# Optimization experiments

Measured on AMD Instinct MI355X. Metric: run time of the kernel, lower is better.

Reference implementation:

```python
import jax, jax.numpy as jnp
import numpy as np

# dims: B batch, N seq, D model_dim, R lora rank, C codebooks, K codebook_input_channel, P kv pairs, M per-codebook output
B, N, D, R, C, K, P = 4, 2048, 1024, 8, 64, 16, 64
M = (D * R) // C  # 128


def setup_inputs() -> dict:
    key = jax.random.key(0)
    ks = jax.random.split(key, 7)
    x = jax.random.normal(ks[0], (B, N, D), dtype=jnp.float32)
    W_A = jax.random.normal(ks[1], (C, K, D), dtype=jnp.float32) * (D ** -0.5)
    emb_A = jax.random.uniform(ks[2], (C, P, K), dtype=jnp.float32, minval=-1.5, maxval=1.5)
    vals_A = jax.random.normal(ks[3], (C, P, M), dtype=jnp.float32)
    W_B = jax.random.normal(ks[4], (C, K, D), dtype=jnp.float32) * (D ** -0.5)
    emb_B = jax.random.uniform(ks[5], (C, P, K), dtype=jnp.float32, minval=-1.5, maxval=1.5)
    vals_B = jax.random.normal(ks[6], (C, P, M), dtype=jnp.float32)
    return {"x": x, "W_A": W_A, "emb_A": emb_A, "vals_A": vals_A,
            "W_B": W_B, "emb_B": emb_B, "vals_B": vals_B}


def _discrete_kv(x, W, emb, vals):
    # x: [B,N,D]; W: [C,K,D] (Linear weight per codebook); emb: [C,P,K]; vals: [C,P,M]
    proj = jnp.einsum('bnd,ckd->cbnk', x, W)  # per-codebook linear projection
    # squared euclidean distance to each key (argmin is same as cdist argmin)
    d2 = (jnp.sum(proj * proj, axis=-1, keepdims=True)
          - 2.0 * jnp.einsum('cbnk,cpk->cbnp', proj, emb)
          + jnp.sum(emb * emb, axis=-1)[:, None, None, :])  # [C,B,N,P]
    idx = jnp.argmin(d2, axis=-1)                      # [C,B,N]
    y = jax.vmap(lambda v, i: v[i])(vals, idx)          # [C,B,N,M]
    # concat over codebooks on last dim -> [B,N,C*M], then view as [B,N,R,D]
    return jnp.transpose(y, (1, 2, 0, 3)).reshape(x.shape[0], x.shape[1], R, D)


def reference(x, W_A, emb_A, vals_A, W_B, emb_B, vals_B):
    A = _discrete_kv(x, W_A, emb_A, vals_A)   # [B,N,R,D]
    Bm = _discrete_kv(x, W_B, emb_B, vals_B)  # [B,N,R,D]
    t = jnp.einsum('bnd,bnrd->bnr', x, A)
    return jnp.einsum('bnr,bnrd->bnd', t, Bm)
```

## Files before the change

kernel.cpp:

```cpp
#include <hip/hip_runtime.h>

#define NTOK   8192
#define DMODEL 1024
#define NC     64
#define NK     16
#define NP     64
#define NM     128
#define LCAP   (1 << 18)
#define MARGIN 2e-3f

typedef _Float16 f16x8  __attribute__((ext_vector_type(8)));
typedef float    f32x16 __attribute__((ext_vector_type(16)));

#define AS1 __attribute__((address_space(1)))
#define AS3 __attribute__((address_space(3)))

__device__ __forceinline__ void glds16(const void* g, void* l) {
    __builtin_amdgcn_global_load_lds((const AS1 void*)g, (AS3 void*)l, 16, 0, 0);
}

__global__ __launch_bounds__(256) void k_split(
    const float* __restrict__ x, const float* __restrict__ W_A, const float* __restrict__ W_B,
    short* __restrict__ xh, short* __restrict__ xl,
    short* __restrict__ whA, short* __restrict__ wlA,
    short* __restrict__ whB, short* __restrict__ wlB)
{
    const int t = blockIdx.x * 256 + threadIdx.x;
    const int NX = 128 * NTOK;
    const int NW = 128 * 1024;

    const float* src;
    short *dh, *dl;
    if (t < NX) {
        const int chunk = t >> 13, tok = t & 8191;
        src = x + (size_t)tok * DMODEL + chunk * 8;
        dh = xh + (size_t)t * 8;  dl = xl + (size_t)t * 8;
    } else if (t < NX + NW) {
        const int u = t - NX, chunk = u >> 10, ck = u & 1023;
        src = W_A + (size_t)ck * DMODEL + chunk * 8;
        dh = whA + (size_t)u * 8; dl = wlA + (size_t)u * 8;
    } else {
        const int u = t - NX - NW, chunk = u >> 10, ck = u & 1023;
        src = W_B + (size_t)ck * DMODEL + chunk * 8;
        dh = whB + (size_t)u * 8; dl = wlB + (size_t)u * 8;
    }

    const float4 a = *(const float4*)src;
    const float4 b = *(const float4*)(src + 4);
    const float v[8] = {a.x, a.y, a.z, a.w, b.x, b.y, b.z, b.w};
    unsigned h[8], l[8];
    #pragma unroll
    for (int j = 0; j < 8; ++j) {
        const _Float16 hf = (_Float16)v[j];
        const _Float16 lf = (_Float16)(v[j] - (float)hf);
        h[j] = (unsigned)__builtin_bit_cast(unsigned short, hf);
        l[j] = (unsigned)__builtin_bit_cast(unsigned short, lf);
    }
    *(int4*)dh = make_int4((int)(h[0] | (h[1] << 16)), (int)(h[2] | (h[3] << 16)),
                           (int)(h[4] | (h[5] << 16)), (int)(h[6] | (h[7] << 16)));
    *(int4*)dl = make_int4((int)(l[0] | (l[1] << 16)), (int)(l[2] | (l[3] << 16)),
                           (int)(l[4] | (l[5] << 16)), (int)(l[6] | (l[7] << 16)));
}

__global__ __launch_bounds__(512, 1) void k_mfma_argmin(
    const short* __restrict__ xh, const short* __restrict__ xl,
    const short* __restrict__ whA, const short* __restrict__ wlA,
    const short* __restrict__ whB, const short* __restrict__ wlB,
    const float* __restrict__ emb_A, const float* __restrict__ emb_B,
    int* __restrict__ idxbuf, int* __restrict__ list, int* __restrict__ cnt)
{
    __shared__ __align__(16) float smem[32768];
    short* ls = (short*)smem;
    float* projT = smem;
    float* embS  = smem + 16640;
    float* e2S   = smem + 24832;

    const int tid = threadIdx.x;
    const int bid = blockIdx.x;
    const int swz = (bid & 7) * 32 + (bid >> 3);
    const int tb  = swz >> 3;
    const int ot  = swz & 7;
    const int set = ot >> 2;
    const short* __restrict__ wh = set ? whB : whA;
    const short* __restrict__ wl = set ? wlB : wlA;
    const float* __restrict__ Ep = set ? emb_B : emb_A;
    const int ckbase = (ot & 3) * 256;

    const int lane = tid & 63;
    const int wid  = tid >> 6;
    const int wr   = wid >> 2;
    const int wc   = wid & 3;
    const int lr31 = lane & 31;
    const int lk2  = lane >> 5;

    f32x16 acc[4][2];
    #pragma unroll
    for (int m = 0; m < 4; ++m)
        #pragma unroll
        for (int n = 0; n < 2; ++n)
            #pragma unroll
            for (int r = 0; r < 16; ++r) acc[m][n][r] = 0.f;

    const size_t oA = ((size_t)(tid >> 8) * NTOK + tb * 256 + (tid & 255)) * 8;
    const size_t oB = ((size_t)(tid >> 8) * 1024 + ckbase + (tid & 255)) * 8;

    #define STAGE(buf, st)                                                   \
        do {                                                                 \
            const size_t sa_ = (size_t)(st) * (size_t)(2 * NTOK * 8);        \
            const size_t sb_ = (size_t)(st) * (size_t)(2 * 1024 * 8);        \
            short* lb_ = ls + (buf) * 16384 + tid * 8;                       \
            glds16(xh + oA + sa_, lb_);                                      \
            glds16(xl + oA + sa_, lb_ + 4096);                               \
            glds16(wh + oB + sb_, lb_ + 8192);                               \
            glds16(wl + oB + sb_, lb_ + 12288);                              \
        } while (0)

    const int aoff = (lk2 * 256 + wr * 128 + lr31) * 8;
    const int boff = 8192 + (lk2 * 256 + wc * 64 + lr31) * 8;

    STAGE(0, 0);
    STAGE(1, 1);
    STAGE(2, 2);

    for (int t = 0; t < 64; ++t) {
        asm volatile("s_waitcnt vmcnt(8)" ::: "memory");
        __builtin_amdgcn_s_barrier();

        const short* bb = ls + (t & 3) * 16384;
        f16x8 ah[4], al[4], bh[2], bl[2];
        #pragma unroll
        for (int m = 0; m < 4; ++m) {
            ah[m] = *(const f16x8*)(bb + aoff + m * 256);
            al[m] = *(const f16x8*)(bb + 4096 + aoff + m * 256);
        }
        #pragma unroll
        for (int n = 0; n < 2; ++n) {
            bh[n] = *(const f16x8*)(bb + boff + n * 256);
            bl[n] = *(const f16x8*)(bb + 8192 - 8192 + 12288 - 12288 + 4096 + boff + n * 256);
        }

        {
            const int ts = (t + 3 < 64) ? (t + 3) : 63;
            STAGE((t + 3) & 3, ts);
        }

        asm volatile("s_waitcnt lgkmcnt(0)" ::: "memory");
        __builtin_amdgcn_sched_barrier(0);
        __builtin_amdgcn_s_setprio(1);
        #pragma unroll
        for (int m = 0; m < 4; ++m)
            #pragma unroll
            for (int n = 0; n < 2; ++n) {
                acc[m][n] = __builtin_amdgcn_mfma_f32_32x32x16_f16(ah[m], bh[n], acc[m][n], 0, 0, 0);
                acc[m][n] = __builtin_amdgcn_mfma_f32_32x32x16_f16(ah[m], bl[n], acc[m][n], 0, 0, 0);
                acc[m][n] = __builtin_amdgcn_mfma_f32_32x32x16_f16(al[m], bh[n], acc[m][n], 0, 0, 0);
            }
        __builtin_amdgcn_s_setprio(0);
    }
    #undef STAGE

    asm volatile("s_waitcnt vmcnt(0)" ::: "memory");
    __builtin_amdgcn_s_barrier();

    #pragma unroll
    for (int ch = 0; ch < 2; ++ch) {
        __syncthreads();
        {
            const float4* eg = (const float4*)(Ep + (size_t)((ot & 3) * 16 + ch * 8) * NP * NK);
            float4* es = (float4*)embS;
            #pragma unroll
            for (int i = 0; i < 4; ++i) es[tid + 512 * i] = eg[tid + 512 * i];
        }
        __syncthreads();
        {
            const float* e = embS + tid * 16;
            float s = 0.f;
            #pragma unroll
            for (int k = 0; k < 16; ++k) s = fmaf(e[k], e[k], s);
            e2S[tid] = s;
        }
        #pragma unroll
        for (int c = 0; c < 4; ++c) {
            __syncthreads();
            if (wr == (c >> 1)) {
                #pragma unroll
                for (int mi = 0; mi < 2; ++mi) {
                    const int m = (c & 1) * 2 + mi;
                    #pragma unroll
                    for (int n = 0; n < 2; ++n) {
                        const int col = wc * 64 + n * 32 + lr31;
                        #pragma unroll
                        for (int r = 0; r < 16; ++r) {
                            const int trow = mi * 32 + (r & 3) + 8 * (r >> 2) + 4 * lk2;
                            projT[col * 65 + trow] = acc[m][n][r];
                        }
                    }
                }
            }
            __syncthreads();
            {
                const int lt = tid & 63, cbl = tid >> 6;
                float pr[16];
                #pragma unroll
                for (int k = 0; k < 16; ++k)
                    pr[k] = projT[((ch * 8 + cbl) * 16 + k) * 65 + lt];
                const float4* eb4 = (const float4*)(embS + cbl * 1024);
                const float* e2 = e2S + cbl * 64;
                float best = 1e30f, second = 1e30f;
                int bp = 0;
                for (int p = 0; p < 64; ++p) {
                    const float4 e0 = eb4[p * 4 + 0], e1 = eb4[p * 4 + 1];
                    const float4 e2v = eb4[p * 4 + 2], e3 = eb4[p * 4 + 3];
                    float s = 0.f;
                    s = fmaf(pr[0], e0.x, s);   s = fmaf(pr[1], e0.y, s);
                    s = fmaf(pr[2], e0.z, s);   s = fmaf(pr[3], e0.w, s);
                    s = fmaf(pr[4], e1.x, s);   s = fmaf(pr[5], e1.y, s);
                    s = fmaf(pr[6], e1.z, s);   s = fmaf(pr[7], e1.w, s);
                    s = fmaf(pr[8], e2v.x, s);  s = fmaf(pr[9], e2v.y, s);
                    s = fmaf(pr[10], e2v.z, s); s = fmaf(pr[11], e2v.w, s);
                    s = fmaf(pr[12], e3.x, s);  s = fmaf(pr[13], e3.y, s);
                    s = fmaf(pr[14], e3.z, s);  s = fmaf(pr[15], e3.w, s);
                    const float g = fmaf(-2.f, s, e2[p]);
                    if (g < best) { second = best; best = g; bp = p; }
                    else if (g < second) { second = g; }
                }
                const int cbook = (ot & 3) * 16 + ch * 8 + cbl;
                const int gtok = tb * 256 + c * 64 + lt;
                idxbuf[(set * NC + cbook) * NTOK + gtok] = bp;
                if (second - best < MARGIN) {
                    const int slot = atomicAdd(cnt, 1);
                    if (slot < LCAP) list[slot] = (set << 19) | (cbook << 13) | gtok;
                }
            }
        }
    }
}

__global__ __launch_bounds__(256) void k_refine(
    const float* __restrict__ x,
    const float* __restrict__ W_A, const float* __restrict__ W_B,
    const float* __restrict__ emb_A, const float* __restrict__ emb_B,
    const int* __restrict__ list, const int* __restrict__ cnt,
    int* __restrict__ idxbuf)
{
    int n = *cnt;
    if (n > LCAP) n = LCAP;
    const int lane = threadIdx.x & 63;
    const int wave = (int)((blockIdx.x * blockDim.x + threadIdx.x) >> 6);
    const int nw   = (int)((gridDim.x * blockDim.x) >> 6);

    for (int i = wave; i < n; i += nw) {
        const int code = list[i];
        const int tok = code & 8191;
        const int c   = (code >> 13) & 63;
        const int set = (code >> 19) & 1;
        const float* __restrict__ Wp = set ? W_B : W_A;
        const float* __restrict__ Ep = set ? emb_B : emb_A;

        double pk[16];
        #pragma unroll
        for (int k = 0; k < 16; ++k) pk[k] = 0.0;
        for (int dd = 0; dd < 16; ++dd) {
            const int d = dd * 64 + lane;
            const double xv = (double)x[(size_t)tok * DMODEL + d];
            #pragma unroll
            for (int k = 0; k < 16; ++k)
                pk[k] = fma(xv, (double)Wp[(size_t)(c * 16 + k) * DMODEL + d], pk[k]);
        }
        #pragma unroll
        for (int k = 0; k < 16; ++k) {
            #pragma unroll
            for (int off = 32; off; off >>= 1)
                pk[k] += __shfl_xor(pk[k], off, 64);
        }
        double d2 = 0.0;
        #pragma unroll
        for (int k = 0; k < 16; ++k) {
            const double t = pk[k] - (double)Ep[(size_t)(c * NP + lane) * NK + k];
            d2 = fma(t, t, d2);
        }
        int bp = lane;
        double bv = d2;
        #pragma unroll
        for (int off = 32; off; off >>= 1) {
            const double ov = __shfl_xor(bv, off, 64);
            const int    op = __shfl_xor(bp, off, 64);
            if (ov < bv || (ov == bv && op < bp)) { bv = ov; bp = op; }
        }
        if (lane == 0) idxbuf[(set * NC + c) * NTOK + tok] = bp;
    }
}

__global__ __launch_bounds__(256) void k_combine(
    const float* __restrict__ x,
    const float* __restrict__ vals_A, const float* __restrict__ vals_B,
    const int* __restrict__ idxbuf, float* __restrict__ out)
{
    __shared__ float xsh[1032];
    __shared__ float part[256];
    __shared__ float tsh[8];
    __shared__ int sIA[64];
    __shared__ int sIB[64];

    const int tid = threadIdx.x;
    const int tok = blockIdx.x;

    if (tid < 64) {
        sIA[tid] = idxbuf[tid * NTOK + tok];
        sIB[tid] = idxbuf[(NC + tid) * NTOK + tok];
    }
    {
        const float4 v = *(const float4*)(x + (size_t)tok * DMODEL + tid * 4);
        const int base = tid * 4 + (tid >> 5);
        xsh[base + 0] = v.x;
        xsh[base + 1] = v.y;
        xsh[base + 2] = v.z;
        xsh[base + 3] = v.w;
    }
    __syncthreads();
    {
        const int c = tid & 63, mseg = tid >> 6;
        const int ia = sIA[c];
        const float4* va = (const float4*)(vals_A + (size_t)(c * NP + ia) * NM + mseg * 32);
        const float* xb = xsh + (c & 7) * 129 + mseg * 32;
        float s = 0.f;
        #pragma unroll
        for (int i = 0; i < 8; ++i) {
            const float4 v = va[i];
            s = fmaf(v.x, xb[i * 4 + 0], s);
            s = fmaf(v.y, xb[i * 4 + 1], s);
            s = fmaf(v.z, xb[i * 4 + 2], s);
            s = fmaf(v.w, xb[i * 4 + 3], s);
        }
        part[tid] = s;
    }
    __syncthreads();
    if (tid < 8) {
        float s = 0.f;
        #pragma unroll
        for (int m = 0; m < 4; ++m)
            #pragma unroll
            for (int j = 0; j < 8; ++j)
                s += part[m * 64 + tid * 8 + j];
        tsh[tid] = s;
    }
    __syncthreads();
    {
        const int d0 = tid * 4, dblk = tid >> 5, dm = d0 & 127;
        float o0 = 0.f, o1 = 0.f, o2 = 0.f, o3 = 0.f;
        #pragma unroll
        for (int r = 0; r < 8; ++r) {
            const int cb = 8 * r + dblk;
            const int ib = sIB[cb];
            const float4 v = *(const float4*)(vals_B + (size_t)(cb * NP + ib) * NM + dm);
            const float tv = tsh[r];
            o0 = fmaf(tv, v.x, o0);
            o1 = fmaf(tv, v.y, o1);
            o2 = fmaf(tv, v.z, o2);
            o3 = fmaf(tv, v.w, o3);
        }
        *(float4*)(out + (size_t)tok * DMODEL + d0) = make_float4(o0, o1, o2, o3);
    }
}

extern "C" void kernel_launch(void* const* d_in, const int* in_sizes, int n_in,
                              void* d_out, int out_size, void* d_ws, size_t ws_size,
                              hipStream_t stream)
{
    const float* x      = (const float*)d_in[0];
    const float* W_A    = (const float*)d_in[1];
    const float* emb_A  = (const float*)d_in[2];
    const float* vals_A = (const float*)d_in[3];
    const float* W_B    = (const float*)d_in[4];
    const float* emb_B  = (const float*)d_in[5];
    const float* vals_B = (const float*)d_in[6];
    float* out = (float*)d_out;

    char* w = (char*)d_ws;
    int*   cnt    = (int*)w;
    int*   list   = (int*)(w + 16);
    int*   idxbuf = (int*)(w + 16 + sizeof(int) * (size_t)LCAP);
    size_t off = 16 + sizeof(int) * (size_t)LCAP + sizeof(int) * (size_t)(2 * NC * NTOK);
    short* xh  = (short*)(w + off); off += (size_t)NTOK * DMODEL * 2;
    short* xl  = (short*)(w + off); off += (size_t)NTOK * DMODEL * 2;
    short* whA = (short*)(w + off); off += (size_t)1024 * DMODEL * 2;
    short* wlA = (short*)(w + off); off += (size_t)1024 * DMODEL * 2;
    short* whB = (short*)(w + off); off += (size_t)1024 * DMODEL * 2;
    short* wlB = (short*)(w + off);

    hipMemsetAsync(cnt, 0, sizeof(int), stream);
    k_split<<<5120, 256, 0, stream>>>(x, W_A, W_B, xh, xl, whA, wlA, whB, wlB);
    k_mfma_argmin<<<256, 512, 0, stream>>>(xh, xl, whA, wlA, whB, wlB,
                                           emb_A, emb_B, idxbuf, list, cnt);
    k_refine<<<1024, 256, 0, stream>>>(x, W_A, W_B, emb_A, emb_B, list, cnt, idxbuf);
    k_combine<<<NTOK, 256, 0, stream>>>(x, vals_A, vals_B, idxbuf, out);
}
```

Measured before the change: 242.4 us.

## Double-buffer MFMA register fragments and deepen LDS prefetch to four stages

Restructures the GEMM main loop so the LDS fragment loads for step t+1 go into a second register set while the MFMAs for step t run. The global-to-LDS prefetch now runs four stages deep instead of three. The MFMA issue order is regrouped so consecutive instructions hit different accumulators, and the argmin search loop gets unroll 4. The aim is to hide LDS read latency and cut dependent-MFMA stalls, at the cost of more registers and more complex wait/barrier ordering.

```diff
diff --git a/kernel.cpp b/kernel.cpp
--- a/kernel.cpp
+++ b/kernel.cpp
@@ -62,6 +62,40 @@
                            (int)(l[4] | (l[5] << 16)), (int)(l[6] | (l[7] << 16)));
 }
 
+struct Frags { f16x8 ah[4], al[4], bh[2], bl[2]; };
+
+__device__ __forceinline__ void load_frags(Frags& f, const short* bb,
+                                           int aoff, int boff) {
+    #pragma unroll
+    for (int m = 0; m < 4; ++m) {
+        f.ah[m] = *(const f16x8*)(bb + aoff + m * 256);
+        f.al[m] = *(const f16x8*)(bb + 4096 + aoff + m * 256);
+    }
+    #pragma unroll
+    for (int n = 0; n < 2; ++n) {
+        f.bh[n] = *(const f16x8*)(bb + boff + n * 256);
+        f.bl[n] = *(const f16x8*)(bb + 4096 + boff + n * 256);
+    }
+}
+
+__device__ __forceinline__ void do_mfma(f32x16 acc[4][2], const Frags& f) {
+    #pragma unroll
+    for (int m = 0; m < 4; ++m)
+        #pragma unroll
+        for (int n = 0; n < 2; ++n)
+            acc[m][n] = __builtin_amdgcn_mfma_f32_32x32x16_f16(f.ah[m], f.bh[n], acc[m][n], 0, 0, 0);
+    #pragma unroll
+    for (int m = 0; m < 4; ++m)
+        #pragma unroll
+        for (int n = 0; n < 2; ++n)
+            acc[m][n] = __builtin_amdgcn_mfma_f32_32x32x16_f16(f.ah[m], f.bl[n], acc[m][n], 0, 0, 0);
+    #pragma unroll
+    for (int m = 0; m < 4; ++m)
+        #pragma unroll
+        for (int n = 0; n < 2; ++n)
+            acc[m][n] = __builtin_amdgcn_mfma_f32_32x32x16_f16(f.al[m], f.bh[n], acc[m][n], 0, 0, 0);
+}
+
 __global__ __launch_bounds__(512, 1) void k_mfma_argmin(
     const short* __restrict__ xh, const short* __restrict__ xl,
     const short* __restrict__ whA, const short* __restrict__ wlA,
@@ -118,45 +152,44 @@
     const int aoff = (lk2 * 256 + wr * 128 + lr31) * 8;
     const int boff = 8192 + (lk2 * 256 + wc * 64 + lr31) * 8;
 
+    Frags fE, fO;
+
     STAGE(0, 0);
     STAGE(1, 1);
     STAGE(2, 2);
-
-    for (int t = 0; t < 64; ++t) {
-        asm volatile("s_waitcnt vmcnt(8)" ::: "memory");
-        __builtin_amdgcn_s_barrier();
-
-        const short* bb = ls + (t & 3) * 16384;
-        f16x8 ah[4], al[4], bh[2], bl[2];
-        #pragma unroll
-        for (int m = 0; m < 4; ++m) {
-            ah[m] = *(const f16x8*)(bb + aoff + m * 256);
-            al[m] = *(const f16x8*)(bb + 4096 + aoff + m * 256);
-        }
-        #pragma unroll
-        for (int n = 0; n < 2; ++n) {
-            bh[n] = *(const f16x8*)(bb + boff + n * 256);
-            bl[n] = *(const f16x8*)(bb + 8192 - 8192 + 12288 - 12288 + 4096 + boff + n * 256);
-        }
-
-        {
-            const int ts = (t + 3 < 64) ? (t + 3) : 63;
-            STAGE((t + 3) & 3, ts);
-        }
-
-        asm volatile("s_waitcnt lgkmcnt(0)" ::: "memory");
-        __builtin_amdgcn_sched_barrier(0);
-        __builtin_amdgcn_s_setprio(1);
-        #pragma unroll
-        for (int m = 0; m < 4; ++m)
-            #pragma unroll
-            for (int n = 0; n < 2; ++n) {
-                acc[m][n] = __builtin_amdgcn_mfma_f32_32x32x16_f16(ah[m], bh[n], acc[m][n], 0, 0, 0);
-                acc[m][n] = __builtin_amdgcn_mfma_f32_32x32x16_f16(ah[m], bl[n], acc[m][n], 0, 0, 0);
-                acc[m][n] = __builtin_amdgcn_mfma_f32_32x32x16_f16(al[m], bh[n], acc[m][n], 0, 0, 0);
-            }
-        __builtin_amdgcn_s_setprio(0);
-    }
+    STAGE(3, 3);
+    asm volatile("s_waitcnt vmcnt(12)" ::: "memory");
+    __builtin_amdgcn_s_barrier();
+    __builtin_amdgcn_sched_barrier(0);
+    load_frags(fE, ls, aoff, boff);
+
+    #define BODY(T, CUR, NXT)                                                \
+        do {                                                                 \
+            asm volatile("s_waitcnt vmcnt(8)" ::: "memory");                 \
+            asm volatile("s_waitcnt lgkmcnt(0)" ::: "memory");               \
+            __builtin_amdgcn_sched_barrier(0);                               \
+            __builtin_amdgcn_s_barrier();                                    \
+            __builtin_amdgcn_sched_barrier(0);                               \
+            load_frags(NXT, ls + (((T) + 1) & 3) * 16384, aoff, boff);       \
+            { const int ts_ = ((T) + 4 < 64) ? (T) + 4 : 63;                 \
+              STAGE((T) & 3, ts_); }                                         \
+            __builtin_amdgcn_s_setprio(1);                                   \
+            do_mfma(acc, CUR);                                               \
+            __builtin_amdgcn_s_setprio(0);                                   \
+        } while (0)
+
+    for (int t = 0; t < 62; t += 2) {
+        BODY(t, fE, fO);
+        BODY(t + 1, fO, fE);
+    }
+    BODY(62, fE, fO);
+    asm volatile("s_waitcnt lgkmcnt(0)" ::: "memory");
+    __builtin_amdgcn_sched_barrier(0);
+    __builtin_amdgcn_s_barrier();
+    __builtin_amdgcn_s_setprio(1);
+    do_mfma(acc, fO);
+    __builtin_amdgcn_s_setprio(0);
+    #undef BODY
     #undef STAGE
 
     asm volatile("s_waitcnt vmcnt(0)" ::: "memory");
@@ -208,6 +241,7 @@
                 const float* e2 = e2S + cbl * 64;
                 float best = 1e30f, second = 1e30f;
                 int bp = 0;
+                #pragma unroll 4
                 for (int p = 0; p < 64; ++p) {
                     const float4 e0 = eb4[p * 4 + 0], e1 = eb4[p * 4 + 1];
                     const float4 e2v = eb4[p * 4 + 2], e3 = eb4[p * 4 + 3];
```

After: 240.6 us. No clear change (-0.8%).
